# Kernel tuning notes

Measured on AMD Instinct MI355X. Metric: run time of the kernel, lower is better.

The kernel has to match this reference:

```python
import jax, jax.numpy as jnp
import numpy as np

B, N, M = 4, 512, 8192
QUERY_DIM, INPUT_DIM = 512, 256
HEADS, DIM_HEAD = 8, 64
ATT_DIM = HEADS * DIM_HEAD  # 512


def setup_inputs() -> dict:
    key = jax.random.key(0)
    ks = jax.random.split(key, 6)
    x = jax.random.normal(ks[0], (B, N, QUERY_DIM), dtype=jnp.float32)
    context = jax.random.normal(ks[1], (B, M, INPUT_DIM), dtype=jnp.float32)
    # Linear weights stored as [in, out] for x @ W
    Wq = jax.random.normal(ks[2], (QUERY_DIM, ATT_DIM), dtype=jnp.float32) / np.sqrt(QUERY_DIM)
    Wkv = jax.random.normal(ks[3], (INPUT_DIM, 2 * ATT_DIM), dtype=jnp.float32) / np.sqrt(INPUT_DIM)
    Wo = jax.random.normal(ks[4], (ATT_DIM, QUERY_DIM), dtype=jnp.float32) / np.sqrt(ATT_DIM)
    bo = jax.random.normal(ks[5], (QUERY_DIM,), dtype=jnp.float32) * 0.01
    return {"x": x, "context": context, "Wq": Wq, "Wkv": Wkv, "Wo": Wo, "bo": bo}


def reference(x, context, Wq, Wkv, Wo, bo):
    scale = DIM_HEAD ** -0.5
    q = x @ Wq                      # [B, N, H*D]
    kv = context @ Wkv              # [B, M, 2*H*D]
    k, v = jnp.split(kv, 2, axis=-1)
    # split heads: b n (h d) -> b h n d
    q = q.reshape(B, N, HEADS, DIM_HEAD).transpose(0, 2, 1, 3)
    k = k.reshape(B, M, HEADS, DIM_HEAD).transpose(0, 2, 1, 3)
    v = v.reshape(B, M, HEADS, DIM_HEAD).transpose(0, 2, 1, 3)
    scores = jnp.einsum('bhid,bhjd->bhij', q, k) * scale  # [B, H, N, M]
    attn = jax.nn.softmax(scores, axis=-1)
    out = jnp.einsum('bhij,bhjd->bhid', attn, v)           # [B, H, N, D]
    out = out.transpose(0, 2, 1, 3).reshape(B, N, ATT_DIM)
    return out @ Wo + bo
```

## Files before the change

kernel.cpp:

```cpp
#include <hip/hip_runtime.h>
#include <hip/hip_bf16.h>
#include <cstdint>

#define NB 4
#define NQ 512
#define NM 8192
#define NH 8
#define DH 64

typedef short bf16x8s __attribute__((ext_vector_type(8)));
typedef float f32x4  __attribute__((ext_vector_type(4)));

static __device__ __forceinline__ short f2bs(float f) {
    __hip_bfloat16 h = __float2bfloat16(f);
    return *reinterpret_cast<short*>(&h);
}
static __device__ __forceinline__ unsigned pk2(float a, float b) {
    unsigned lo = (unsigned)(unsigned short)f2bs(a);
    unsigned hi = (unsigned)(unsigned short)f2bs(b);
    return lo | (hi << 16);
}

__global__ __launch_bounds__(256) void gemm_proj(
    const float* __restrict__ A, const float* __restrict__ W,
    float* __restrict__ C, const float* __restrict__ bias)
{
    __shared__ __align__(16) short As[64 * 72];
    __shared__ __align__(16) short Bs[64 * 72];

    const int t  = threadIdx.x;
    const int tm = blockIdx.x >> 3;
    const int tn = blockIdx.x & 7;
    const int w  = t >> 6, ln = t & 63;
    const int m16 = ln & 15, quad = ln >> 4;
    const int wm = w & 1, wn = w >> 1;

    const int ar = t >> 2, akq = (t & 3) << 4;
    const int bn = t & 63, bkh = (t >> 6) << 4;
    const float* Ap = A + (size_t)(tm * 64 + ar) * 512 + akq;
    const float* Bp = W + (size_t)bkh * 512 + tn * 64 + bn;

    f32x4 acc[2][2] = {};

    for (int k0 = 0; k0 < 512; k0 += 64) {
        float4 a0 = *(const float4*)(Ap + k0);
        float4 a1 = *(const float4*)(Ap + k0 + 4);
        float4 a2 = *(const float4*)(Ap + k0 + 8);
        float4 a3 = *(const float4*)(Ap + k0 + 12);
        float bv[16];
        #pragma unroll
        for (int kk = 0; kk < 16; ++kk)
            bv[kk] = Bp[(size_t)(k0 + kk) * 512];

        __syncthreads();
        {
            uint4 w0 = { pk2(a0.x,a0.y), pk2(a0.z,a0.w), pk2(a1.x,a1.y), pk2(a1.z,a1.w) };
            uint4 w1 = { pk2(a2.x,a2.y), pk2(a2.z,a2.w), pk2(a3.x,a3.y), pk2(a3.z,a3.w) };
            *(uint4*)&As[ar * 72 + akq]     = w0;
            *(uint4*)&As[ar * 72 + akq + 8] = w1;
            uint4 v0 = { pk2(bv[0],bv[1]),  pk2(bv[2],bv[3]),   pk2(bv[4],bv[5]),   pk2(bv[6],bv[7]) };
            uint4 v1 = { pk2(bv[8],bv[9]),  pk2(bv[10],bv[11]), pk2(bv[12],bv[13]), pk2(bv[14],bv[15]) };
            *(uint4*)&Bs[bn * 72 + bkh]     = v0;
            *(uint4*)&Bs[bn * 72 + bkh + 8] = v1;
        }
        __syncthreads();

        #pragma unroll
        for (int ks = 0; ks < 2; ++ks) {
            bf16x8s af[2], bfr[2];
            #pragma unroll
            for (int i = 0; i < 2; ++i)
                af[i] = *(const bf16x8s*)&As[(wm * 32 + i * 16 + m16) * 72 + ks * 32 + quad * 8];
            #pragma unroll
            for (int j = 0; j < 2; ++j)
                bfr[j] = *(const bf16x8s*)&Bs[(wn * 32 + j * 16 + m16) * 72 + ks * 32 + quad * 8];
            #pragma unroll
            for (int i = 0; i < 2; ++i)
                #pragma unroll
                for (int j = 0; j < 2; ++j)
                    acc[i][j] = __builtin_amdgcn_mfma_f32_16x16x32_bf16(af[i], bfr[j], acc[i][j], 0, 0, 0);
        }
    }

    const int row0 = tm * 64 + wm * 32;
    const int col0 = tn * 64 + wn * 32;
    #pragma unroll
    for (int j = 0; j < 2; ++j) {
        const int col = col0 + j * 16 + m16;
        const float bb = bias ? bias[col] : 0.f;
        #pragma unroll
        for (int i = 0; i < 2; ++i)
            #pragma unroll
            for (int r = 0; r < 4; ++r)
                C[(size_t)(row0 + i * 16 + quad * 4 + r) * 512 + col] = acc[i][j][r] + bb;
    }
}

__global__ __launch_bounds__(256) void gemm_kv(
    const float* __restrict__ A,
    const float* __restrict__ Bw,
    short* __restrict__ Kf, short* __restrict__ Vf)
{
    __shared__ __align__(16) short As[128 * 40];
    __shared__ __align__(16) short Bs[128 * 40];

    const int t  = threadIdx.x;
    const int tm = blockIdx.x & 255, tn = blockIdx.x >> 8;
    const int w  = t >> 6, ln = t & 63;
    const int m16 = ln & 15, quad = ln >> 4;
    const int wm = w & 1, wn = w >> 1;

    const int ar = t >> 3;
    const int ac = (t & 7) << 2;
    const int sb_n = t & 127, sb_kh = (t >> 7) << 4;

    const float* Abase = A  + (size_t)(tm * 128 + ar) * 256 + ac;
    const float* Bbase = Bw + (size_t)sb_kh * 1024 + tn * 128 + sb_n;

    f32x4 acc[4][4] = {};

    for (int k0 = 0; k0 < 256; k0 += 32) {
        float4 av[4];
        #pragma unroll
        for (int p = 0; p < 4; ++p)
            av[p] = *(const float4*)(Abase + (size_t)p * 32 * 256 + k0);
        float bv[16];
        #pragma unroll
        for (int kk = 0; kk < 16; ++kk)
            bv[kk] = Bbase[(size_t)(k0 + kk) * 1024];

        __syncthreads();
        #pragma unroll
        for (int p = 0; p < 4; ++p) {
            uint2 wv = { pk2(av[p].x, av[p].y), pk2(av[p].z, av[p].w) };
            *(uint2*)&As[(p * 32 + ar) * 40 + ac] = wv;
        }
        {
            uint4 v0 = { pk2(bv[0],bv[1]),  pk2(bv[2],bv[3]),   pk2(bv[4],bv[5]),   pk2(bv[6],bv[7]) };
            uint4 v1 = { pk2(bv[8],bv[9]),  pk2(bv[10],bv[11]), pk2(bv[12],bv[13]), pk2(bv[14],bv[15]) };
            *(uint4*)&Bs[sb_n * 40 + sb_kh]     = v0;
            *(uint4*)&Bs[sb_n * 40 + sb_kh + 8] = v1;
        }
        __syncthreads();

        bf16x8s af[4], bfr[4];
        #pragma unroll
        for (int i = 0; i < 4; ++i)
            af[i] = *(const bf16x8s*)&As[(wm * 64 + i * 16 + m16) * 40 + quad * 8];
        #pragma unroll
        for (int j = 0; j < 4; ++j)
            bfr[j] = *(const bf16x8s*)&Bs[(wn * 64 + j * 16 + m16) * 40 + quad * 8];
        #pragma unroll
        for (int i = 0; i < 4; ++i)
            #pragma unroll
            for (int j = 0; j < 4; ++j)
                acc[i][j] = __builtin_amdgcn_mfma_f32_16x16x32_bf16(af[i], bfr[j], acc[i][j], 0, 0, 0);
    }

    const int col0 = tn * 128 + wn * 64;
    const int row0 = tm * 128 + wm * 64;
    const int b    = row0 >> 13;
    const int mr0  = row0 & (NM - 1);

    if (col0 < 512) {
        const int h = col0 >> 6;
        short* Kp = Kf + (size_t)(b * NH + h) * (NM * DH);
        #pragma unroll
        for (int i = 0; i < 4; ++i)
            #pragma unroll
            for (int j = 0; j < 4; ++j) {
                const int d = j * 16 + m16;
                #pragma unroll
                for (int r = 0; r < 4; ++r) {
                    const int key = mr0 + i * 16 + quad * 4 + r;
                    const int idx = ((key >> 4) * 2 + (d >> 5)) * 512
                                  + (((d >> 3) & 3) * 16 + (key & 15)) * 8 + (d & 7);
                    Kp[idx] = f2bs(acc[i][j][r]);
                }
            }
    } else {
        const int h = (col0 - 512) >> 6;
        short* Vp = Vf + (size_t)(b * NH + h) * (NM * DH);
        #pragma unroll
        for (int i = 0; i < 4; ++i)
            #pragma unroll
            for (int j = 0; j < 4; ++j) {
                const int key0 = mr0 + i * 16 + quad * 4;
                const int idx = (j * 256 + (key0 >> 5)) * 512
                              + ((((key0 >> 3) & 3) * 16 + m16) * 8) + (key0 & 7);
                uint2 pk;
                pk.x = pk2(acc[i][j][0], acc[i][j][1]);
                pk.y = pk2(acc[i][j][2], acc[i][j][3]);
                *(uint2*)(Vp + idx) = pk;
            }
    }
}

__global__ __launch_bounds__(256) void attn_mfma(
    const float* __restrict__ Q,
    const short* __restrict__ Kfr,
    const short* __restrict__ Vfr,
    float* __restrict__ Og)
{
    __shared__ __align__(16) float Obuf[4 * 32 * 68];
    __shared__ float lbuf[4 * 32];

    const int bid = blockIdx.x;
    const int xcd = bid & 7, grp = bid >> 3;
    const int bh  = xcd * 4 + (grp & 3);
    const int qt  = grp >> 2;
    const int b   = bh >> 3, h = bh & 7;
    const int t   = threadIdx.x;
    const int w   = t >> 6, ln = t & 63;
    const int m16 = ln & 15, quad = ln >> 4;

    const short* Kbase = Kfr + (size_t)bh * (NM * DH);
    const short* Vbase = Vfr + (size_t)bh * (NM * DH);

    bf16x8s qf[2][2];
    #pragma unroll
    for (int mt = 0; mt < 2; ++mt) {
        const float* qrow = Q + ((size_t)(b * NQ + qt * 32 + mt * 16 + m16)) * 512 + h * 64;
        #pragma unroll
        for (int ks = 0; ks < 2; ++ks) {
            float4 x0 = *(const float4*)(qrow + ks * 32 + quad * 8);
            float4 x1 = *(const float4*)(qrow + ks * 32 + quad * 8 + 4);
            bf16x8s f;
            f[0] = f2bs(x0.x * 0.125f); f[1] = f2bs(x0.y * 0.125f);
            f[2] = f2bs(x0.z * 0.125f); f[3] = f2bs(x0.w * 0.125f);
            f[4] = f2bs(x1.x * 0.125f); f[5] = f2bs(x1.y * 0.125f);
            f[6] = f2bs(x1.z * 0.125f); f[7] = f2bs(x1.w * 0.125f);
            qf[mt][ks] = f;
        }
    }

    f32x4 o[2][4] = {};
    float lpr[2] = {0.f, 0.f};

    const int srcLo = (((quad << 1) & 3) << 4) + m16;
    const int srcHi = ((((quad << 1) + 1) & 3) << 4) + m16;
    const bool ktHi = quad >= 2;

    bf16x8s kf[4][2];
    {
        const int kc = w * 64;
        #pragma unroll
        for (int nt = 0; nt < 4; ++nt)
            #pragma unroll
            for (int ks = 0; ks < 2; ++ks)
                kf[nt][ks] = *(const bf16x8s*)(Kbase + ((((kc >> 4) + nt) * 2 + ks) << 9) + ln * 8);
    }

    for (int it = 0; it < 32; ++it) {
        const int kc = it * 256 + w * 64;

        bf16x8s vf[4][2];
        #pragma unroll
        for (int dt = 0; dt < 4; ++dt)
            #pragma unroll
            for (int ks = 0; ks < 2; ++ks)
                vf[dt][ks] = *(const bf16x8s*)(Vbase + ((dt * 256 + (kc >> 5) + ks) << 9) + ln * 8);

        f32x4 st[2][4] = {};
        #pragma unroll
        for (int kt = 0; kt < 4; ++kt)
            #pragma unroll
            for (int mt = 0; mt < 2; ++mt) {
                st[mt][kt] = __builtin_amdgcn_mfma_f32_16x16x32_bf16(kf[kt][0], qf[mt][0], st[mt][kt], 0, 0, 0);
                st[mt][kt] = __builtin_amdgcn_mfma_f32_16x16x32_bf16(kf[kt][1], qf[mt][1], st[mt][kt], 0, 0, 0);
            }

        if (it + 1 < 32) {
            const int kn = (it + 1) * 256 + w * 64;
            #pragma unroll
            for (int nt = 0; nt < 4; ++nt)
                #pragma unroll
                for (int ks = 0; ks < 2; ++ks)
                    kf[nt][ks] = *(const bf16x8s*)(Kbase + ((((kn >> 4) + nt) * 2 + ks) << 9) + ln * 8);
        }

        unsigned pp[2][4][2];
        #pragma unroll
        for (int mt = 0; mt < 2; ++mt)
            #pragma unroll
            for (int kt = 0; kt < 4; ++kt) {
                const float p0 = __expf(st[mt][kt][0]);
                const float p1 = __expf(st[mt][kt][1]);
                const float p2 = __expf(st[mt][kt][2]);
                const float p3 = __expf(st[mt][kt][3]);
                lpr[mt] += (p0 + p1) + (p2 + p3);
                pp[mt][kt][0] = pk2(p0, p1);
                pp[mt][kt][1] = pk2(p2, p3);
            }

        #pragma unroll
        for (int mt = 0; mt < 2; ++mt)
            #pragma unroll
            for (int ks = 0; ks < 2; ++ks) {
                const unsigned a0 = __shfl(pp[mt][2 * ks][0], srcLo);
                const unsigned b0 = __shfl(pp[mt][2 * ks + 1][0], srcLo);
                const unsigned a1 = __shfl(pp[mt][2 * ks][1], srcLo);
                const unsigned b1 = __shfl(pp[mt][2 * ks + 1][1], srcLo);
                const unsigned a2 = __shfl(pp[mt][2 * ks][0], srcHi);
                const unsigned b2 = __shfl(pp[mt][2 * ks + 1][0], srcHi);
                const unsigned a3 = __shfl(pp[mt][2 * ks][1], srcHi);
                const unsigned b3 = __shfl(pp[mt][2 * ks + 1][1], srcHi);
                uint4 pb;
                pb.x = ktHi ? b0 : a0;
                pb.y = ktHi ? b1 : a1;
                pb.z = ktHi ? b2 : a2;
                pb.w = ktHi ? b3 : a3;
                bf16x8s pbv = *reinterpret_cast<bf16x8s*>(&pb);
                #pragma unroll
                for (int dt = 0; dt < 4; ++dt)
                    o[mt][dt] = __builtin_amdgcn_mfma_f32_16x16x32_bf16(vf[dt][ks], pbv, o[mt][dt], 0, 0, 0);
            }
    }

    float lf[2];
    #pragma unroll
    for (int mt = 0; mt < 2; ++mt) {
        float l = lpr[mt];
        l += __shfl_xor(l, 16);
        l += __shfl_xor(l, 32);
        lf[mt] = l;
    }

    #pragma unroll
    for (int mt = 0; mt < 2; ++mt)
        #pragma unroll
        for (int dt = 0; dt < 4; ++dt)
            *(f32x4*)&Obuf[(w * 32 + mt * 16 + m16) * 68 + dt * 16 + quad * 4] = o[mt][dt];
    if (quad == 0) {
        lbuf[w * 32 +      m16] = lf[0];
        lbuf[w * 32 + 16 + m16] = lf[1];
    }
    __syncthreads();
    {
        const int row = t >> 3, d0 = (t & 7) << 3;
        const float l = lbuf[row] + lbuf[32 + row] + lbuf[64 + row] + lbuf[96 + row];
        const float inv = 1.0f / l;
        float res[8];
        #pragma unroll
        for (int j = 0; j < 8; ++j) {
            float a = Obuf[(row) * 68 + d0 + j]
                    + Obuf[(32 + row) * 68 + d0 + j]
                    + Obuf[(64 + row) * 68 + d0 + j]
                    + Obuf[(96 + row) * 68 + d0 + j];
            res[j] = a * inv;
        }
        float* op = Og + ((size_t)(b * NQ + qt * 32 + row)) * 512 + h * 64 + d0;
        float4 r0 = {res[0], res[1], res[2], res[3]};
        float4 r1 = {res[4], res[5], res[6], res[7]};
        *(float4*)op = r0;
        *(float4*)(op + 4) = r1;
    }
}

extern "C" void kernel_launch(void* const* d_in, const int* in_sizes, int n_in,
                              void* d_out, int out_size, void* d_ws, size_t ws_size,
                              hipStream_t stream) {
    (void)in_sizes; (void)n_in; (void)out_size; (void)ws_size;

    const float* x   = (const float*)d_in[0];
    const float* ctx = (const float*)d_in[1];
    const float* Wq  = (const float*)d_in[2];
    const float* Wkv = (const float*)d_in[3];
    const float* Wo  = (const float*)d_in[4];
    const float* bo  = (const float*)d_in[5];
    float* out = (float*)d_out;

    float* ws    = (float*)d_ws;
    float* q     = ws;
    float* attno = q + (size_t)2048 * 512;
    short* Kf    = (short*)(attno + (size_t)2048 * 512);
    short* Vf    = Kf + (size_t)NB * NH * NM * DH;

    gemm_proj<<<dim3(256), dim3(256), 0, stream>>>(x, Wq, q, nullptr);

    gemm_kv<<<dim3(2048), dim3(256), 0, stream>>>(ctx, Wkv, Kf, Vf);

    attn_mfma<<<dim3(512), dim3(256), 0, stream>>>(q, Kf, Vf, attno);

    gemm_proj<<<dim3(256), dim3(256), 0, stream>>>(attno, Wo, out, bo);
}
```

Measured before the change: 209.7 us.

## Merge Q and KV projections into one launch, shrink proj tiles, cheaper bf16 pack

Merges the Q projection and the KV projection into a single kernel that dispatches on block index, removing one launch and letting the small Q GEMM overlap with the KV GEMM. The projection GEMM tile is reduced from 64x64 to 32x64, doubling its block count to 512 for better occupancy on the small output projection. The float-to-bf16 conversion is replaced with an add-and-truncate round plus a byte-permute pack. This rounding is round-half-up rather than round-to-nearest-even and does not handle NaN, and the smaller tiles re-read the weights more often.

```diff
diff --git a/kernel.cpp b/kernel.cpp
--- a/kernel.cpp
+++ b/kernel.cpp
@@ -12,41 +12,39 @@
 typedef float f32x4  __attribute__((ext_vector_type(4)));
 
 static __device__ __forceinline__ short f2bs(float f) {
-    __hip_bfloat16 h = __float2bfloat16(f);
-    return *reinterpret_cast<short*>(&h);
+    unsigned u = __builtin_bit_cast(unsigned, f);
+    return (short)(unsigned short)((u + 0x8000u) >> 16);
 }
 static __device__ __forceinline__ unsigned pk2(float a, float b) {
-    unsigned lo = (unsigned)(unsigned short)f2bs(a);
-    unsigned hi = (unsigned)(unsigned short)f2bs(b);
-    return lo | (hi << 16);
-}
-
-__global__ __launch_bounds__(256) void gemm_proj(
+    unsigned au = __builtin_bit_cast(unsigned, a) + 0x8000u;
+    unsigned bu = __builtin_bit_cast(unsigned, b) + 0x8000u;
+    return __builtin_amdgcn_perm(bu, au, 0x07060302u);
+}
+
+__device__ __forceinline__ void proj32_body(
     const float* __restrict__ A, const float* __restrict__ W,
-    float* __restrict__ C, const float* __restrict__ bias)
-{
-    __shared__ __align__(16) short As[64 * 72];
-    __shared__ __align__(16) short Bs[64 * 72];
-
-    const int t  = threadIdx.x;
-    const int tm = blockIdx.x >> 3;
-    const int tn = blockIdx.x & 7;
-    const int w  = t >> 6, ln = t & 63;
+    float* __restrict__ C, const float* __restrict__ bias,
+    int tm, int tn, char* smemraw)
+{
+    short* As = (short*)smemraw;
+    short* Bs = As + 32 * 72;
+
+    const int t = threadIdx.x;
+    const int w = t >> 6, ln = t & 63;
     const int m16 = ln & 15, quad = ln >> 4;
-    const int wm = w & 1, wn = w >> 1;
-
-    const int ar = t >> 2, akq = (t & 3) << 4;
+    const int wm = w >> 1, wn = w & 1;
+
+    const int ar = t >> 3, ac = (t & 7) << 3;
     const int bn = t & 63, bkh = (t >> 6) << 4;
-    const float* Ap = A + (size_t)(tm * 64 + ar) * 512 + akq;
+
+    const float* Ap = A + (size_t)(tm * 32 + ar) * 512 + ac;
     const float* Bp = W + (size_t)bkh * 512 + tn * 64 + bn;
 
-    f32x4 acc[2][2] = {};
+    f32x4 acc[2] = {};
 
     for (int k0 = 0; k0 < 512; k0 += 64) {
         float4 a0 = *(const float4*)(Ap + k0);
         float4 a1 = *(const float4*)(Ap + k0 + 4);
-        float4 a2 = *(const float4*)(Ap + k0 + 8);
-        float4 a3 = *(const float4*)(Ap + k0 + 12);
         float bv[16];
         #pragma unroll
         for (int kk = 0; kk < 16; ++kk)
@@ -54,10 +52,8 @@
 
         __syncthreads();
         {
-            uint4 w0 = { pk2(a0.x,a0.y), pk2(a0.z,a0.w), pk2(a1.x,a1.y), pk2(a1.z,a1.w) };
-            uint4 w1 = { pk2(a2.x,a2.y), pk2(a2.z,a2.w), pk2(a3.x,a3.y), pk2(a3.z,a3.w) };
-            *(uint4*)&As[ar * 72 + akq]     = w0;
-            *(uint4*)&As[ar * 72 + akq + 8] = w1;
+            uint4 wa = { pk2(a0.x,a0.y), pk2(a0.z,a0.w), pk2(a1.x,a1.y), pk2(a1.z,a1.w) };
+            *(uint4*)&As[ar * 72 + ac] = wa;
             uint4 v0 = { pk2(bv[0],bv[1]),  pk2(bv[2],bv[3]),   pk2(bv[4],bv[5]),   pk2(bv[6],bv[7]) };
             uint4 v1 = { pk2(bv[8],bv[9]),  pk2(bv[10],bv[11]), pk2(bv[12],bv[13]), pk2(bv[14],bv[15]) };
             *(uint4*)&Bs[bn * 72 + bkh]     = v0;
@@ -67,45 +63,37 @@
 
         #pragma unroll
         for (int ks = 0; ks < 2; ++ks) {
-            bf16x8s af[2], bfr[2];
-            #pragma unroll
-            for (int i = 0; i < 2; ++i)
-                af[i] = *(const bf16x8s*)&As[(wm * 32 + i * 16 + m16) * 72 + ks * 32 + quad * 8];
-            #pragma unroll
-            for (int j = 0; j < 2; ++j)
-                bfr[j] = *(const bf16x8s*)&Bs[(wn * 32 + j * 16 + m16) * 72 + ks * 32 + quad * 8];
-            #pragma unroll
-            for (int i = 0; i < 2; ++i)
-                #pragma unroll
-                for (int j = 0; j < 2; ++j)
-                    acc[i][j] = __builtin_amdgcn_mfma_f32_16x16x32_bf16(af[i], bfr[j], acc[i][j], 0, 0, 0);
-        }
-    }
-
-    const int row0 = tm * 64 + wm * 32;
+            bf16x8s af = *(const bf16x8s*)&As[(wm * 16 + m16) * 72 + ks * 32 + quad * 8];
+            #pragma unroll
+            for (int nt = 0; nt < 2; ++nt) {
+                bf16x8s bf = *(const bf16x8s*)&Bs[(wn * 32 + nt * 16 + m16) * 72 + ks * 32 + quad * 8];
+                acc[nt] = __builtin_amdgcn_mfma_f32_16x16x32_bf16(af, bf, acc[nt], 0, 0, 0);
+            }
+        }
+    }
+
+    const int row0 = tm * 32 + wm * 16 + quad * 4;
     const int col0 = tn * 64 + wn * 32;
     #pragma unroll
-    for (int j = 0; j < 2; ++j) {
-        const int col = col0 + j * 16 + m16;
+    for (int nt = 0; nt < 2; ++nt) {
+        const int col = col0 + nt * 16 + m16;
         const float bb = bias ? bias[col] : 0.f;
         #pragma unroll
-        for (int i = 0; i < 2; ++i)
-            #pragma unroll
-            for (int r = 0; r < 4; ++r)
-                C[(size_t)(row0 + i * 16 + quad * 4 + r) * 512 + col] = acc[i][j][r] + bb;
-    }
-}
-
-__global__ __launch_bounds__(256) void gemm_kv(
-    const float* __restrict__ A,
-    const float* __restrict__ Bw,
-    short* __restrict__ Kf, short* __restrict__ Vf)
-{
-    __shared__ __align__(16) short As[128 * 40];
-    __shared__ __align__(16) short Bs[128 * 40];
+        for (int r = 0; r < 4; ++r)
+            C[(size_t)(row0 + r) * 512 + col] = acc[nt][r] + bb;
+    }
+}
+
+__device__ __forceinline__ void kv_body(
+    const float* __restrict__ A, const float* __restrict__ Bw,
+    short* __restrict__ Kf, short* __restrict__ Vf,
+    int bid, char* smemraw)
+{
+    short* As = (short*)smemraw;
+    short* Bs = As + 128 * 40;
 
     const int t  = threadIdx.x;
-    const int tm = blockIdx.x & 255, tn = blockIdx.x >> 8;
+    const int tm = bid & 255, tn = bid >> 8;
     const int w  = t >> 6, ln = t & 63;
     const int m16 = ln & 15, quad = ln >> 4;
     const int wm = w & 1, wn = w >> 1;
@@ -196,6 +184,26 @@
     }
 }
 
+__global__ __launch_bounds__(256) void gemm_kvq(
+    const float* __restrict__ x,   const float* __restrict__ Wq, float* __restrict__ q,
+    const float* __restrict__ ctx, const float* __restrict__ Wkv,
+    short* __restrict__ Kf, short* __restrict__ Vf)
+{
+    __shared__ __align__(16) char smem[20480];
+    if (blockIdx.x < 512)
+        proj32_body(x, Wq, q, nullptr, (int)(blockIdx.x >> 3), (int)(blockIdx.x & 7), smem);
+    else
+        kv_body(ctx, Wkv, Kf, Vf, (int)(blockIdx.x - 512), smem);
+}
+
+__global__ __launch_bounds__(256) void gemm_proj32(
+    const float* __restrict__ A, const float* __restrict__ W,
+    float* __restrict__ C, const float* __restrict__ bias)
+{
+    __shared__ __align__(16) char smem[(32 + 64) * 72 * 2];
+    proj32_body(A, W, C, bias, (int)(blockIdx.x >> 3), (int)(blockIdx.x & 7), smem);
+}
+
 __global__ __launch_bounds__(256) void attn_mfma(
     const float* __restrict__ Q,
     const short* __restrict__ Kfr,
@@ -225,12 +233,9 @@
         for (int ks = 0; ks < 2; ++ks) {
             float4 x0 = *(const float4*)(qrow + ks * 32 + quad * 8);
             float4 x1 = *(const float4*)(qrow + ks * 32 + quad * 8 + 4);
-            bf16x8s f;
-            f[0] = f2bs(x0.x * 0.125f); f[1] = f2bs(x0.y * 0.125f);
-            f[2] = f2bs(x0.z * 0.125f); f[3] = f2bs(x0.w * 0.125f);
-            f[4] = f2bs(x1.x * 0.125f); f[5] = f2bs(x1.y * 0.125f);
-            f[6] = f2bs(x1.z * 0.125f); f[7] = f2bs(x1.w * 0.125f);
-            qf[mt][ks] = f;
+            uint4 pkv = { pk2(x0.x * 0.125f, x0.y * 0.125f), pk2(x0.z * 0.125f, x0.w * 0.125f),
+                          pk2(x1.x * 0.125f, x1.y * 0.125f), pk2(x1.z * 0.125f, x1.w * 0.125f) };
+            qf[mt][ks] = *reinterpret_cast<bf16x8s*>(&pkv);
         }
     }
 
@@ -376,11 +381,9 @@
     short* Kf    = (short*)(attno + (size_t)2048 * 512);
     short* Vf    = Kf + (size_t)NB * NH * NM * DH;
 
-    gemm_proj<<<dim3(256), dim3(256), 0, stream>>>(x, Wq, q, nullptr);
-
-    gemm_kv<<<dim3(2048), dim3(256), 0, stream>>>(ctx, Wkv, Kf, Vf);
+    gemm_kvq<<<dim3(2560), dim3(256), 0, stream>>>(x, Wq, q, ctx, Wkv, Kf, Vf);
 
     attn_mfma<<<dim3(512), dim3(256), 0, stream>>>(q, Kf, Vf, attno);
 
-    gemm_proj<<<dim3(256), dim3(256), 0, stream>>>(attno, Wo, out, bo);
-}
+    gemm_proj32<<<dim3(512), dim3(256), 0, stream>>>(attno, Wo, out, bo);
+}
```

Result: faster. 205.3 us (-2.1%).
